# Kernel optimization log

Hardware: AMD Instinct MI355X
Metric: run time of the kernel (lower is better)

The kernel has to match this reference:

```python
import jax, jax.numpy as jnp
import numpy as np

N = 500_000            # nodes
E = 16_000_000         # used edges (var edges); E_total = 2*E
EPS = 1e-5             # BatchNorm eps
SQRT_C = np.sqrt(2.0).astype(np.float32)  # out_channels=2


def setup_inputs() -> dict:
    key = jax.random.key(0)
    ks = jax.random.split(key, 20)
    w = lambda k, s: (jax.random.normal(k, s, jnp.float32) * 0.5)
    d = {}
    d["x"] = jax.random.normal(ks[0], (N, 2), jnp.float32)
    d["edge_index"] = jax.random.randint(ks[1], (2, 2 * E), 0, N, jnp.int32)
    d["edge_attr"] = jax.random.normal(ks[2], (2 * E, 2), jnp.float32)
    d["mask"] = (jax.random.uniform(ks[3], (N,)) < 0.5).astype(jnp.float32)
    # TransformerConv(2,2,edge_dim=2,heads=1) params
    d["Wq"], d["bq"] = w(ks[4], (2, 2)), w(ks[5], (2,))
    d["Wk"], d["bk"] = w(ks[6], (2, 2)), w(ks[7], (2,))
    d["Wv"], d["bv"] = w(ks[8], (2, 2)), w(ks[9], (2,))
    d["We"] = w(ks[10], (2, 2))               # lin_edge, bias=False
    d["Wskip"], d["bskip"] = w(ks[11], (2, 2)), w(ks[12], (2,))
    # BatchNorm(2) affine params
    d["gamma"], d["beta"] = jnp.ones((2,), jnp.float32), jnp.zeros((2,), jnp.float32)
    # final Linear(2,1)
    d["Wf"], d["bf"] = w(ks[13], (1, 2)), w(ks[14], (1,))
    return d


def _transformer_conv(x, src, dst, ea, Wq, bq, Wk, bk, Wv, bv, We, Wskip, bskip):
    # PyG TransformerConv, heads=1, concat=True, root_weight=True, beta=False
    q = x @ Wq.T + bq                       # [N,2]
    k = x @ Wk.T + bk                       # [N,2]
    v = x @ Wv.T + bv                       # [N,2]
    e = ea @ We.T                           # [E,2]
    k_j = k[src] + e                        # [E,2]
    alpha = jnp.sum(q[dst] * k_j, axis=1) / SQRT_C  # [E]
    # segment softmax over destination nodes
    m = jax.ops.segment_max(alpha, dst, num_segments=N)          # -inf for empty
    m = jnp.where(jnp.isfinite(m), m, 0.0)
    a = jnp.exp(alpha - m[dst])
    s = jax.ops.segment_sum(a, dst, num_segments=N)
    wgt = a / jnp.where(s[dst] > 0, s[dst], 1.0)                 # [E]
    msg = (v[src] + e) * wgt[:, None]                            # [E,2]
    out = jax.ops.segment_sum(msg, dst, num_segments=N)          # [N,2]
    return out + x @ Wskip.T + bskip


def _neighbor_max(x, src, dst, ea_clause):
    # vectorized form of the per-node Python loop (scatter-max)
    s = jnp.sum(x[src] * ea_clause, axis=1)                      # [E]
    seg = jax.ops.segment_max(s, dst, num_segments=N)            # [N]
    deg = jax.ops.segment_sum(jnp.ones_like(s), dst, num_segments=N)
    has = deg > 0
    mx = jnp.where(has, seg, 0.0)
    stacked = jnp.stack([mx, 1.0 - mx], axis=1)                  # [N,2]
    return jnp.where(has[:, None], stacked, x)


def reference(x, edge_index, edge_attr, mask, Wq, bq, Wk, bk, Wv, bv, We,
              Wskip, bskip, gamma, beta, Wf, bf):
    ei = edge_index[:, 1::2]        # var_index = odd columns
    ea = edge_attr[1::2]            # var edge attrs
    ea_clause = edge_attr[0::2]     # clause edge attrs
    src, dst = ei[0], ei[1]
    h = _transformer_conv(x, src, dst, ea, Wq, bq, Wk, bk, Wv, bv, We, Wskip, bskip)
    # BatchNorm1d, training-mode batch statistics (biased var)
    mu = jnp.mean(h, axis=0)
    var = jnp.mean((h - mu) ** 2, axis=0)
    h = (h - mu) / jnp.sqrt(var + EPS) * gamma + beta
    # softmax over node dim (dim=0)
    h = jax.nn.softmax(h, axis=0)
    h = _neighbor_max(h, src, dst, ea_clause)
    # iterations=1 -> extra loop body does not execute
    out = jnp.squeeze(h @ Wf.T + bf)       # [N]
    return out * mask
```

## Files before the change

### kernel.cpp

```cpp
#include <hip/hip_runtime.h>
#include <hip/hip_fp16.h>

#define NNODES 500000
#define NEDGES 16000000
#define NBLK 1024
#define EPB (NEDGES / NBLK)
#define BSH 11
#define BSZ 2048
#define NBKT 245
#define BDIM 256
#define CHUNK 2048
#define KPC (CHUNK / 256)
#define CTH 1024

typedef unsigned long long u64;
typedef unsigned int u32;
typedef unsigned short u16;


__device__ __forceinline__ u32 fmap_ord(float x) {
    u32 u = __float_as_uint(x);
    return (u & 0x80000000u) ? ~u : (u | 0x80000000u);
}
__device__ __forceinline__ float funmap_ord(u32 u) {
    u32 bits = (u & 0x80000000u) ? (u ^ 0x80000000u) : ~u;
    return __uint_as_float(bits);
}

__device__ __forceinline__ void block_reduce_atomic4(float v0, float v1, float v2, float v3,
                                                     float* dst) {
    for (int off = 32; off > 0; off >>= 1) {
        v0 += __shfl_down(v0, off, 64);
        v1 += __shfl_down(v1, off, 64);
        v2 += __shfl_down(v2, off, 64);
        v3 += __shfl_down(v3, off, 64);
    }
    __shared__ float red[4][4];
    int lane = threadIdx.x & 63, wid = threadIdx.x >> 6;
    if (lane == 0) { red[wid][0] = v0; red[wid][1] = v1; red[wid][2] = v2; red[wid][3] = v3; }
    __syncthreads();
    if (threadIdx.x < 4) {
        float t = red[0][threadIdx.x] + red[1][threadIdx.x] + red[2][threadIdx.x] + red[3][threadIdx.x];
        unsafeAtomicAdd(&dst[threadIdx.x], t);
    }
}

__device__ __forceinline__ void block_reduce_atomic4_w16(float v0, float v1, float v2, float v3,
                                                         float* dst) {
    for (int off = 32; off > 0; off >>= 1) {
        v0 += __shfl_down(v0, off, 64);
        v1 += __shfl_down(v1, off, 64);
        v2 += __shfl_down(v2, off, 64);
        v3 += __shfl_down(v3, off, 64);
    }
    __shared__ float red[16][4];
    int lane = threadIdx.x & 63, wid = threadIdx.x >> 6;
    if (lane == 0) { red[wid][0] = v0; red[wid][1] = v1; red[wid][2] = v2; red[wid][3] = v3; }
    __syncthreads();
    if (threadIdx.x < 4) {
        float t = 0.f;
        #pragma unroll
        for (int w = 0; w < 16; ++w) t += red[w][threadIdx.x];
        unsafeAtomicAdd(&dst[threadIdx.x], t);
    }
}


__global__ __launch_bounds__(64) void k_zero_accum(float* accum) {
    if (threadIdx.x < 16) accum[threadIdx.x] = 0.f;
}

__global__ __launch_bounds__(256) void k_node_prep(
    const float* __restrict__ x,
    const float* __restrict__ Wq, const float* __restrict__ bq,
    const float* __restrict__ Wk, const float* __restrict__ bk,
    const float* __restrict__ Wv, const float* __restrict__ bv,
    float2* __restrict__ q, float4* __restrict__ kv) {
    int i = blockIdx.x * blockDim.x + threadIdx.x;
    if (i >= NNODES) return;
    float2 xv = ((const float2*)x)[i];
    float q0 = fmaf(Wq[0], xv.x, fmaf(Wq[1], xv.y, bq[0]));
    float q1 = fmaf(Wq[2], xv.x, fmaf(Wq[3], xv.y, bq[1]));
    float k0 = fmaf(Wk[0], xv.x, fmaf(Wk[1], xv.y, bk[0]));
    float k1 = fmaf(Wk[2], xv.x, fmaf(Wk[3], xv.y, bk[1]));
    float v0 = fmaf(Wv[0], xv.x, fmaf(Wv[1], xv.y, bv[0]));
    float v1 = fmaf(Wv[2], xv.x, fmaf(Wv[3], xv.y, bv[1]));
    q[i] = make_float2(q0, q1);
    kv[i] = make_float4(k0, k1, v0, v1);
}

__global__ void k_ln_final(const float* __restrict__ gamma, const float* __restrict__ beta,
                           float* __restrict__ accum) {
    float n = (float)NNODES;
    float mu0 = accum[0] / n, mu1 = accum[1] / n;
    float var0 = accum[2] / n - mu0 * mu0;
    float var1 = accum[3] / n - mu1 * mu1;
    float sc0 = gamma[0] * rsqrtf(var0 + 1e-5f);
    float sc1 = gamma[1] * rsqrtf(var1 + 1e-5f);
    accum[8] = sc0;
    accum[9] = sc1;
    accum[10] = beta[0] - mu0 * sc0;
    accum[11] = beta[1] - mu1 * sc1;
}

__global__ __launch_bounds__(256) void k_softmax(
    const float2* __restrict__ h, float2* __restrict__ pp, float* __restrict__ accum) {
    int i = blockIdx.x * blockDim.x + threadIdx.x;
    float p0 = 0.f, p1 = 0.f;
    if (i < NNODES) {
        float sc0 = accum[8], sc1 = accum[9], sh0 = accum[10], sh1 = accum[11];
        float2 hv = h[i];
        p0 = __expf(fmaf(hv.x, sc0, sh0));
        p1 = __expf(fmaf(hv.y, sc1, sh1));
        pp[i] = make_float2(p0, p1);
    }
    block_reduce_atomic4(p0, p1, 0.f, 0.f, accum + 4);
}

__global__ void k_sm_final(float* __restrict__ accum) {
    accum[12] = 1.f / accum[4];
    accum[13] = 1.f / accum[5];
}


__global__ __launch_bounds__(256) void k_hist(const int2* __restrict__ dst2, u32* __restrict__ M) {
    __shared__ u32 hist[BDIM];
    if (threadIdx.x < BDIM) hist[threadIdx.x] = 0u;
    __syncthreads();
    int beg = blockIdx.x * EPB, end = beg + EPB;
    #pragma unroll 4
    for (int e = beg + threadIdx.x; e < end; e += 256)
        atomicAdd(&hist[dst2[e].y >> BSH], 1u);
    __syncthreads();
    u32* row = M + (size_t)blockIdx.x * BDIM;
    if (threadIdx.x < BDIM) row[threadIdx.x] = hist[threadIdx.x];
}

__global__ __launch_bounds__(256) void k_bucket_prefix(u32* __restrict__ M, u32* __restrict__ bucketTotal) {
    __shared__ u32 col[NBLK];
    int b = blockIdx.x;
    for (int j = threadIdx.x; j < NBLK; j += 256) col[j] = M[(size_t)j * BDIM + b];
    __syncthreads();
    if (threadIdx.x == 0) {
        u32 run = 0;
        for (int j = 0; j < NBLK; ++j) { u32 c = col[j]; col[j] = run; run += c; }
        bucketTotal[b] = run;
    }
    __syncthreads();
    for (int j = threadIdx.x; j < NBLK; j += 256) M[(size_t)j * BDIM + b] = col[j];
}

__global__ __launch_bounds__(256) void k_scan_serial(const u32* __restrict__ bucketTotal,
                                                     u32* __restrict__ bucketBase) {
    __shared__ u32 t[BDIM];
    __shared__ u32 o[BDIM + 1];
    if (threadIdx.x < BDIM) t[threadIdx.x] = bucketTotal[threadIdx.x];
    __syncthreads();
    if (threadIdx.x == 0) {
        u32 run = 0;
        for (int j = 0; j < BDIM; ++j) { o[j] = run; run += t[j]; }
        o[BDIM] = run;
    }
    __syncthreads();
    for (int j = threadIdx.x; j < BDIM + 1; j += 256) bucketBase[j] = o[j];
}


__global__ __launch_bounds__(256) void k_scatter_stg(
    const int2* __restrict__ src2, const int2* __restrict__ dst2,
    const float4* __restrict__ ea4, const float* __restrict__ We,
    const u32* __restrict__ M, const u32* __restrict__ bucketBase,
    float4* __restrict__ R) {
    __shared__ u32 hist[BDIM];
    __shared__ u32 lbase[BDIM];
    __shared__ u32 gcur[BDIM];
    __shared__ u32 wsum[4];
    __shared__ float4 buf[CHUNK];
    __shared__ u16 bkt[CHUNK];

    const u32* row = M + (size_t)blockIdx.x * BDIM;
    if (threadIdx.x < BDIM) gcur[threadIdx.x] = row[threadIdx.x] + bucketBase[threadIdx.x];
    float we00 = We[0], we01 = We[1], we10 = We[2], we11 = We[3];
    int beg = blockIdx.x * EPB;
    int lane = threadIdx.x & 63, wid = threadIdx.x >> 6;

    for (int c0 = 0; c0 < EPB; c0 += CHUNK) {
        int cn = min(CHUNK, EPB - c0);
        if (threadIdx.x < BDIM) hist[threadIdx.x] = 0u;
        __syncthreads();

        float4 recs[KPC]; u32 bks[KPC]; u32 rnk[KPC]; bool val[KPC];
        #pragma unroll
        for (int k = 0; k < KPC; ++k) {
            int tt = k * 256 + threadIdx.x;
            val[k] = tt < cn;
            if (val[k]) {
                int e = beg + c0 + tt;
                int si = src2[e].y;
                int di = dst2[e].y;
                float4 eav = ea4[e];
                float e0 = fmaf(we00, eav.z, we01 * eav.w);
                float e1 = fmaf(we10, eav.z, we11 * eav.w);
                __half2 hc = __floats2half2_rn(eav.x, eav.y);
                u32 b = (u32)di >> BSH;
                u32 idx = (u32)si | ((u32)(di & (BSZ - 1)) << 19);
                recs[k] = make_float4(__uint_as_float(idx), e0, e1,
                                      __uint_as_float(*(u32*)&hc));
                bks[k] = b;
                rnk[k] = atomicAdd(&hist[b], 1u);
            }
        }
        __syncthreads();

        u32 s = hist[threadIdx.x];
        u32 inc = s;
        #pragma unroll
        for (int d = 1; d < 64; d <<= 1) {
            u32 v = __shfl_up(inc, d, 64);
            if (lane >= d) inc += v;
        }
        if (lane == 63) wsum[wid] = inc;
        __syncthreads();
        u32 woff = 0;
        for (int w = 0; w < wid; ++w) woff += wsum[w];
        lbase[threadIdx.x] = woff + inc - s;
        __syncthreads();

        #pragma unroll
        for (int k = 0; k < KPC; ++k) {
            if (val[k]) {
                u32 p = lbase[bks[k]] + rnk[k];
                buf[p] = recs[k];
                bkt[p] = (u16)bks[k];
            }
        }
        __syncthreads();

        for (int j = threadIdx.x; j < cn; j += 256) {
            u32 b = bkt[j];
            R[(size_t)gcur[b] + (u32)j - lbase[b]] = buf[j];
        }
        __syncthreads();

        if (threadIdx.x < BDIM) gcur[threadIdx.x] += hist[threadIdx.x];
        __syncthreads();
    }
}

__global__ __launch_bounds__(CTH) void k_attn16(
    const float4* __restrict__ R,
    const u32* __restrict__ bucketBase, const u32* __restrict__ bucketTotal,
    const float4* __restrict__ kv, const float2* __restrict__ qp,
    const float* __restrict__ x,
    const float* __restrict__ Wskip, const float* __restrict__ bskip,
    float2* __restrict__ h, float* __restrict__ accum) {
    __shared__ float sA[BSZ], m0A[BSZ], m1A[BSZ];
    __shared__ float2 qT[BSZ];
    int b = blockIdx.x, base = b << BSH;
    for (int j = threadIdx.x; j < BSZ; j += CTH) {
        sA[j] = 0.f; m0A[j] = 0.f; m1A[j] = 0.f;
        int i = base + j;
        qT[j] = (i < NNODES) ? qp[i] : make_float2(0.f, 0.f);
    }
    __syncthreads();
    int beg = bucketBase[b], end = beg + bucketTotal[b];
    for (int idx = beg + threadIdx.x; idx < end; idx += CTH) {
        float4 r = R[idx];
        u32 rec = __float_as_uint(r.x);
        int si = rec & 0x7FFFFu;
        int li = rec >> 19;
        float4 kvv = kv[si];
        float2 qv = qT[li];
        float alpha = fmaf(qv.x, kvv.x + r.y, qv.y * (kvv.y + r.z)) * 0.70710678118654752f;
        float a = __expf(alpha);
        atomicAdd(&sA[li], a);
        atomicAdd(&m0A[li], a * (kvv.z + r.y));
        atomicAdd(&m1A[li], a * (kvv.w + r.z));
    }
    __syncthreads();
    float r0 = 0.f, r1 = 0.f, r2 = 0.f, r3 = 0.f;
    float w00 = Wskip[0], w01 = Wskip[1], w10 = Wskip[2], w11 = Wskip[3];
    float c0 = bskip[0], c1 = bskip[1];
    for (int j = threadIdx.x; j < BSZ; j += CTH) {
        int i = base + j;
        if (i < NNODES) {
            float2 xv = ((const float2*)x)[i];
            float s = sA[j];
            float inv = s > 0.f ? 1.f / s : 0.f;
            float h0 = fmaf(m0A[j], inv, fmaf(w00, xv.x, fmaf(w01, xv.y, c0)));
            float h1 = fmaf(m1A[j], inv, fmaf(w10, xv.x, fmaf(w11, xv.y, c1)));
            h[i] = make_float2(h0, h1);
            r0 += h0; r1 += h1; r2 += h0 * h0; r3 += h1 * h1;
        }
    }
    block_reduce_atomic4_w16(r0, r1, r2, r3, accum);
}

__global__ __launch_bounds__(CTH) void k_nmax16(
    const float4* __restrict__ R,
    const u32* __restrict__ bucketBase, const u32* __restrict__ bucketTotal,
    const float2* __restrict__ pp, const float* __restrict__ accum,
    const float* __restrict__ Wf, const float* __restrict__ bf,
    const float* __restrict__ mask, float* __restrict__ out) {
    __shared__ u32 mxA[BSZ];
    __shared__ float maskT[BSZ];
    int b = blockIdx.x, base = b << BSH;
    for (int j = threadIdx.x; j < BSZ; j += CTH) {
        mxA[j] = 0u;
        int i = base + j;
        maskT[j] = (i < NNODES) ? mask[i] : 0.f;
    }
    __syncthreads();
    float inv0 = accum[12], inv1 = accum[13];
    int beg = bucketBase[b], end = beg + bucketTotal[b];
    for (int idx = beg + threadIdx.x; idx < end; idx += CTH) {
        float4 r = R[idx];
        u32 rec = __float_as_uint(r.x);
        int li = rec >> 19;
        if (maskT[li] == 0.f) continue;
        int si = rec & 0x7FFFFu;
        u32 hcbits = __float_as_uint(r.w);
        __half2 hc = *(__half2*)&hcbits;
        float2 cf = __half22float2(hc);
        float2 pv = pp[si];
        float sE = fmaf(pv.x * inv0, cf.x, pv.y * inv1 * cf.y);
        atomicMax(&mxA[li], fmap_ord(sE));
    }
    __syncthreads();
    float wf0 = Wf[0], wf1 = Wf[1], bb = bf[0];
    for (int j = threadIdx.x; j < BSZ; j += CTH) {
        int i = base + j;
        if (i >= NNODES) continue;
        u32 m = mxA[j];
        float h0, h1;
        if (m != 0u) { float v = funmap_ord(m); h0 = v; h1 = 1.f - v; }
        else { float2 pv = pp[i]; h0 = pv.x * inv0; h1 = pv.y * inv1; }
        out[i] = fmaf(wf0, h0, fmaf(wf1, h1, bb)) * maskT[j];
    }
}


__global__ __launch_bounds__(256) void k_init_f(float* s, float* msg, u32* mxb, float* accum) {
    int i = blockIdx.x * blockDim.x + threadIdx.x;
    if (i < NNODES) { s[i] = 0.f; mxb[i] = 0u; }
    if (i < 2 * NNODES) msg[i] = 0.f;
    if (i < 16) accum[i] = 0.f;
}

__global__ __launch_bounds__(256) void k_edge_attn_f(
    const int* __restrict__ ei, const float* __restrict__ ea,
    const float* __restrict__ We,
    const float2* __restrict__ q, const float4* __restrict__ kv,
    float* __restrict__ s, float* __restrict__ msg) {
    int e = blockIdx.x * blockDim.x + threadIdx.x;
    if (e >= NEDGES) return;
    float we00 = We[0], we01 = We[1], we10 = We[2], we11 = We[3];
    int si = ((const int2*)ei)[e].y;
    int di = ((const int2*)(ei + 2 * NEDGES))[e].y;
    float2 eav = ((const float2*)ea)[2 * e + 1];
    float4 kvv = kv[si];
    float2 qv = q[di];
    float e0 = fmaf(we00, eav.x, we01 * eav.y);
    float e1 = fmaf(we10, eav.x, we11 * eav.y);
    float alpha = fmaf(qv.x, kvv.x + e0, qv.y * (kvv.y + e1)) * 0.70710678118654752f;
    float a = __expf(alpha);
    unsafeAtomicAdd(&s[di], a);
    unsafeAtomicAdd(&msg[2 * di], a * (kvv.z + e0));
    unsafeAtomicAdd(&msg[2 * di + 1], a * (kvv.w + e1));
}

__global__ __launch_bounds__(256) void k_node_h_f(
    const float* __restrict__ x,
    const float* __restrict__ Wskip, const float* __restrict__ bskip,
    const float* __restrict__ s, float* __restrict__ msg, float* __restrict__ accum) {
    int i = blockIdx.x * blockDim.x + threadIdx.x;
    float h0 = 0.f, h1 = 0.f;
    if (i < NNODES) {
        float2 xv = ((const float2*)x)[i];
        float sk0 = fmaf(Wskip[0], xv.x, fmaf(Wskip[1], xv.y, bskip[0]));
        float sk1 = fmaf(Wskip[2], xv.x, fmaf(Wskip[3], xv.y, bskip[1]));
        float sv = s[i];
        float inv = sv > 0.f ? 1.f / sv : 0.f;
        h0 = fmaf(msg[2 * i], inv, sk0);
        h1 = fmaf(msg[2 * i + 1], inv, sk1);
        msg[2 * i] = h0;
        msg[2 * i + 1] = h1;
    }
    block_reduce_atomic4(h0, h1, h0 * h0, h1 * h1, accum);
}

__global__ __launch_bounds__(256) void k_edge_nmax_f(
    const int* __restrict__ ei, const float* __restrict__ ea,
    const float2* __restrict__ pp, const float* __restrict__ accum,
    u32* __restrict__ mxb) {
    int e = blockIdx.x * blockDim.x + threadIdx.x;
    if (e >= NEDGES) return;
    float inv0 = accum[12], inv1 = accum[13];
    int si = ((const int2*)ei)[e].y;
    int di = ((const int2*)(ei + 2 * NEDGES))[e].y;
    float2 c = ((const float2*)ea)[2 * e];
    float2 pv = pp[si];
    float sE = fmaf(pv.x * inv0, c.x, pv.y * inv1 * c.y);
    atomicMax(&mxb[di], fmap_ord(sE));
}

__global__ __launch_bounds__(256) void k_final_f(
    const u32* __restrict__ mxb, const float2* __restrict__ pp,
    const float* __restrict__ accum,
    const float* __restrict__ Wf, const float* __restrict__ bf,
    const float* __restrict__ mask, float* __restrict__ out) {
    int i = blockIdx.x * blockDim.x + threadIdx.x;
    if (i >= NNODES) return;
    u32 m = mxb[i];
    float h0, h1;
    if (m != 0u) {
        float v = funmap_ord(m);
        h0 = v;
        h1 = 1.f - v;
    } else {
        float2 pv = pp[i];
        h0 = pv.x * accum[12];
        h1 = pv.y * accum[13];
    }
    out[i] = fmaf(Wf[0], h0, fmaf(Wf[1], h1, bf[0])) * mask[i];
}


extern "C" void kernel_launch(void* const* d_in, const int* in_sizes, int n_in,
                              void* d_out, int out_size, void* d_ws, size_t ws_size,
                              hipStream_t stream) {
    const float* x     = (const float*)d_in[0];
    const int*   ei    = (const int*)d_in[1];
    const float* ea    = (const float*)d_in[2];
    const float* mask  = (const float*)d_in[3];
    const float* Wq    = (const float*)d_in[4];
    const float* bq    = (const float*)d_in[5];
    const float* Wk    = (const float*)d_in[6];
    const float* bk    = (const float*)d_in[7];
    const float* Wv    = (const float*)d_in[8];
    const float* bv    = (const float*)d_in[9];
    const float* We    = (const float*)d_in[10];
    const float* Wskip = (const float*)d_in[11];
    const float* bskip = (const float*)d_in[12];
    const float* gamma = (const float*)d_in[13];
    const float* beta  = (const float*)d_in[14];
    const float* Wf    = (const float*)d_in[15];
    const float* bf    = (const float*)d_in[16];
    float* out = (float*)d_out;

    const size_t N = NNODES;
    const size_t E = NEDGES;
    const int B = 256;
    const int gridN = (NNODES + B - 1) / B;

    const int2*   src2 = (const int2*)ei;
    const int2*   dst2 = (const int2*)(ei + 2 * NEDGES);
    const float4* ea4  = (const float4*)ea;

    size_t need16 = 16 * N
                  + 16 * E
                  + 8 * N
                  + 8 * N
                  + 8 * N
                  + 4 * (size_t)NBLK * BDIM
                  + 4 * BDIM
                  + 4 * (BDIM + 16)
                  + 64;

    if (ws_size >= need16) {
        char* base = (char*)d_ws;
        float4* kv = (float4*)base;                 base += 16 * N;
        float4* R  = (float4*)base;                 base += 16 * E;
        float2* q  = (float2*)base;                 base += 8 * N;
        float2* h  = (float2*)base;                 base += 8 * N;
        float2* p  = (float2*)base;                 base += 8 * N;
        u32*    M  = (u32*)base;                    base += 4 * (size_t)NBLK * BDIM;
        u32*    bT = (u32*)base;                    base += 4 * BDIM;
        u32*    bB = (u32*)base;                    base += 4 * (BDIM + 16);
        float*  accum = (float*)base;

        k_zero_accum<<<1, 64, 0, stream>>>(accum);
        k_node_prep<<<gridN, B, 0, stream>>>(x, Wq, bq, Wk, bk, Wv, bv, q, kv);
        k_hist<<<NBLK, B, 0, stream>>>(dst2, M);
        k_bucket_prefix<<<BDIM, B, 0, stream>>>(M, bT);
        k_scan_serial<<<1, B, 0, stream>>>(bT, bB);
        k_scatter_stg<<<NBLK, B, 0, stream>>>(src2, dst2, ea4, We, M, bB, R);
        k_attn16<<<NBKT, CTH, 0, stream>>>(R, bB, bT, kv, q, x, Wskip, bskip, h, accum);
        k_ln_final<<<1, 1, 0, stream>>>(gamma, beta, accum);
        k_softmax<<<gridN, B, 0, stream>>>(h, p, accum);
        k_sm_final<<<1, 1, 0, stream>>>(accum);
        k_nmax16<<<NBKT, CTH, 0, stream>>>(R, bB, bT, p, accum, Wf, bf, mask, out);
    } else {
        float*  q   = (float*)d_ws;
        float*  kvf = q + 2 * N;
        float*  s   = kvf + 4 * N;
        float*  msg = s + N;
        u32*    mxb = (u32*)(msg + 2 * N);
        float*  accum = (float*)(mxb + N);
        int grid2N = (int)((2 * N + B - 1) / B);
        int gridE  = (NEDGES + B - 1) / B;

        k_init_f<<<grid2N, B, 0, stream>>>(s, msg, mxb, accum);
        k_node_prep<<<gridN, B, 0, stream>>>(x, Wq, bq, Wk, bk, Wv, bv, (float2*)q, (float4*)kvf);
        k_edge_attn_f<<<gridE, B, 0, stream>>>(ei, ea, We, (const float2*)q, (const float4*)kvf, s, msg);
        k_node_h_f<<<gridN, B, 0, stream>>>(x, Wskip, bskip, s, msg, accum);
        k_ln_final<<<1, 1, 0, stream>>>(gamma, beta, accum);
        k_softmax<<<gridN, B, 0, stream>>>((const float2*)msg, (float2*)q, accum);
        k_sm_final<<<1, 1, 0, stream>>>(accum);
        k_edge_nmax_f<<<gridE, B, 0, stream>>>(ei, ea, (const float2*)q, accum, mxb);
        k_final_f<<<gridN, B, 0, stream>>>(mxb, (const float2*)q, accum, Wf, bf, mask, out);
    }
}
```

Measured before the change: 664.0 us.

## Compute attention weights during scatter and split edge records for nmax pass

The exp-weighted attention terms are now computed per edge in the scatter kernel, which gathers q[dst] and kv[src] itself, and it writes precomputed (a, a*m0, a*m1) records. The attention kernel then only does shared-memory atomic accumulation. A separate 8-byte record array carries the index and half-precision clause attributes, so the neighbor-max pass reads half the bytes. In exchange the scatter kernel does random q gathers over the whole node range instead of a bucket-local shared-memory table, and it writes an extra 8 bytes per edge. The workspace also grows by 8 bytes per edge, which could push execution onto the fallback path if the workspace is small.

Result: slower. 1.015 ms (+52.9%).

```diff
diff --git a/kernel.cpp b/kernel.cpp
--- a/kernel.cpp
+++ b/kernel.cpp
@@ -166,16 +166,18 @@
 }
 
 
-__global__ __launch_bounds__(256) void k_scatter_stg(
+__global__ __launch_bounds__(256) void k_scatter_fused(
     const int2* __restrict__ src2, const int2* __restrict__ dst2,
     const float4* __restrict__ ea4, const float* __restrict__ We,
+    const float2* __restrict__ qp, const float4* __restrict__ kvp,
     const u32* __restrict__ M, const u32* __restrict__ bucketBase,
-    float4* __restrict__ R) {
+    float4* __restrict__ R1, uint2* __restrict__ R2) {
     __shared__ u32 hist[BDIM];
     __shared__ u32 lbase[BDIM];
     __shared__ u32 gcur[BDIM];
     __shared__ u32 wsum[4];
-    __shared__ float4 buf[CHUNK];
+    __shared__ float4 buf1[CHUNK];
+    __shared__ uint2 buf2[CHUNK];
     __shared__ u16 bkt[CHUNK];
 
     const u32* row = M + (size_t)blockIdx.x * BDIM;
@@ -189,7 +191,7 @@
         if (threadIdx.x < BDIM) hist[threadIdx.x] = 0u;
         __syncthreads();
 
-        float4 recs[KPC]; u32 bks[KPC]; u32 rnk[KPC]; bool val[KPC];
+        float4 r1[KPC]; uint2 r2[KPC]; u32 bks[KPC]; u32 rnk[KPC]; bool val[KPC];
         #pragma unroll
         for (int k = 0; k < KPC; ++k) {
             int tt = k * 256 + threadIdx.x;
@@ -201,11 +203,17 @@
                 float4 eav = ea4[e];
                 float e0 = fmaf(we00, eav.z, we01 * eav.w);
                 float e1 = fmaf(we10, eav.z, we11 * eav.w);
+                float4 kvv = kvp[si];
+                float2 qv = qp[di];
+                float alpha = fmaf(qv.x, kvv.x + e0, qv.y * (kvv.y + e1)) * 0.70710678118654752f;
+                float a = __expf(alpha);
+                float am0 = a * (kvv.z + e0);
+                float am1 = a * (kvv.w + e1);
+                u32 b = (u32)di >> BSH;
+                u32 lisi = (u32)si | ((u32)(di & (BSZ - 1)) << 19);
                 __half2 hc = __floats2half2_rn(eav.x, eav.y);
-                u32 b = (u32)di >> BSH;
-                u32 idx = (u32)si | ((u32)(di & (BSZ - 1)) << 19);
-                recs[k] = make_float4(__uint_as_float(idx), e0, e1,
-                                      __uint_as_float(*(u32*)&hc));
+                r1[k] = make_float4(__uint_as_float(lisi), a, am0, am1);
+                r2[k] = make_uint2(lisi, *(u32*)&hc);
                 bks[k] = b;
                 rnk[k] = atomicAdd(&hist[b], 1u);
             }
@@ -230,7 +238,8 @@
         for (int k = 0; k < KPC; ++k) {
             if (val[k]) {
                 u32 p = lbase[bks[k]] + rnk[k];
-                buf[p] = recs[k];
+                buf1[p] = r1[k];
+                buf2[p] = r2[k];
                 bkt[p] = (u16)bks[k];
             }
         }
@@ -238,7 +247,9 @@
 
         for (int j = threadIdx.x; j < cn; j += 256) {
             u32 b = bkt[j];
-            R[(size_t)gcur[b] + (u32)j - lbase[b]] = buf[j];
+            u32 off = gcur[b] + (u32)j - lbase[b];
+            R1[(size_t)off] = buf1[j];
+            R2[(size_t)off] = buf2[j];
         }
         __syncthreads();
 
@@ -248,34 +259,24 @@
 }
 
 __global__ __launch_bounds__(CTH) void k_attn16(
-    const float4* __restrict__ R,
+    const float4* __restrict__ R1,
     const u32* __restrict__ bucketBase, const u32* __restrict__ bucketTotal,
-    const float4* __restrict__ kv, const float2* __restrict__ qp,
     const float* __restrict__ x,
     const float* __restrict__ Wskip, const float* __restrict__ bskip,
     float2* __restrict__ h, float* __restrict__ accum) {
     __shared__ float sA[BSZ], m0A[BSZ], m1A[BSZ];
-    __shared__ float2 qT[BSZ];
     int b = blockIdx.x, base = b << BSH;
     for (int j = threadIdx.x; j < BSZ; j += CTH) {
         sA[j] = 0.f; m0A[j] = 0.f; m1A[j] = 0.f;
-        int i = base + j;
-        qT[j] = (i < NNODES) ? qp[i] : make_float2(0.f, 0.f);
     }
     __syncthreads();
     int beg = bucketBase[b], end = beg + bucketTotal[b];
     for (int idx = beg + threadIdx.x; idx < end; idx += CTH) {
-        float4 r = R[idx];
-        u32 rec = __float_as_uint(r.x);
-        int si = rec & 0x7FFFFu;
-        int li = rec >> 19;
-        float4 kvv = kv[si];
-        float2 qv = qT[li];
-        float alpha = fmaf(qv.x, kvv.x + r.y, qv.y * (kvv.y + r.z)) * 0.70710678118654752f;
-        float a = __expf(alpha);
-        atomicAdd(&sA[li], a);
-        atomicAdd(&m0A[li], a * (kvv.z + r.y));
-        atomicAdd(&m1A[li], a * (kvv.w + r.z));
+        float4 r = R1[idx];
+        int li = (int)(__float_as_uint(r.x) >> 19);
+        atomicAdd(&sA[li], r.y);
+        atomicAdd(&m0A[li], r.z);
+        atomicAdd(&m1A[li], r.w);
     }
     __syncthreads();
     float r0 = 0.f, r1 = 0.f, r2 = 0.f, r3 = 0.f;
@@ -297,7 +298,7 @@
 }
 
 __global__ __launch_bounds__(CTH) void k_nmax16(
-    const float4* __restrict__ R,
+    const uint2* __restrict__ R2,
     const u32* __restrict__ bucketBase, const u32* __restrict__ bucketTotal,
     const float2* __restrict__ pp, const float* __restrict__ accum,
     const float* __restrict__ Wf, const float* __restrict__ bf,
@@ -314,13 +315,11 @@
     float inv0 = accum[12], inv1 = accum[13];
     int beg = bucketBase[b], end = beg + bucketTotal[b];
     for (int idx = beg + threadIdx.x; idx < end; idx += CTH) {
-        float4 r = R[idx];
-        u32 rec = __float_as_uint(r.x);
-        int li = rec >> 19;
+        uint2 r = R2[idx];
+        int li = (int)(r.x >> 19);
         if (maskT[li] == 0.f) continue;
-        int si = rec & 0x7FFFFu;
-        u32 hcbits = __float_as_uint(r.w);
-        __half2 hc = *(__half2*)&hcbits;
+        int si = (int)(r.x & 0x7FFFFu);
+        __half2 hc = *(__half2*)&r.y;
         float2 cf = __half22float2(hc);
         float2 pv = pp[si];
         float sE = fmaf(pv.x * inv0, cf.x, pv.y * inv1 * cf.y);
@@ -457,20 +456,22 @@
     const int2*   dst2 = (const int2*)(ei + 2 * NEDGES);
     const float4* ea4  = (const float4*)ea;
 
-    size_t need16 = 16 * N
-                  + 16 * E
-                  + 8 * N
-                  + 8 * N
-                  + 8 * N
-                  + 4 * (size_t)NBLK * BDIM
-                  + 4 * BDIM
-                  + 4 * (BDIM + 16)
-                  + 64;
-
-    if (ws_size >= need16) {
+    size_t need = 16 * N
+                + 16 * E
+                + 8 * E
+                + 8 * N
+                + 8 * N
+                + 8 * N
+                + 4 * (size_t)NBLK * BDIM
+                + 4 * BDIM
+                + 4 * (BDIM + 16)
+                + 64;
+
+    if (ws_size >= need) {
         char* base = (char*)d_ws;
         float4* kv = (float4*)base;                 base += 16 * N;
-        float4* R  = (float4*)base;                 base += 16 * E;
+        float4* R1 = (float4*)base;                 base += 16 * E;
+        uint2*  R2 = (uint2*)base;                  base += 8 * E;
         float2* q  = (float2*)base;                 base += 8 * N;
         float2* h  = (float2*)base;                 base += 8 * N;
         float2* p  = (float2*)base;                 base += 8 * N;
@@ -484,12 +485,12 @@
         k_hist<<<NBLK, B, 0, stream>>>(dst2, M);
         k_bucket_prefix<<<BDIM, B, 0, stream>>>(M, bT);
         k_scan_serial<<<1, B, 0, stream>>>(bT, bB);
-        k_scatter_stg<<<NBLK, B, 0, stream>>>(src2, dst2, ea4, We, M, bB, R);
-        k_attn16<<<NBKT, CTH, 0, stream>>>(R, bB, bT, kv, q, x, Wskip, bskip, h, accum);
+        k_scatter_fused<<<NBLK, B, 0, stream>>>(src2, dst2, ea4, We, q, kv, M, bB, R1, R2);
+        k_attn16<<<NBKT, CTH, 0, stream>>>(R1, bB, bT, x, Wskip, bskip, h, accum);
         k_ln_final<<<1, 1, 0, stream>>>(gamma, beta, accum);
         k_softmax<<<gridN, B, 0, stream>>>(h, p, accum);
         k_sm_final<<<1, 1, 0, stream>>>(accum);
-        k_nmax16<<<NBKT, CTH, 0, stream>>>(R, bB, bT, p, accum, Wf, bf, mask, out);
+        k_nmax16<<<NBKT, CTH, 0, stream>>>(R2, bB, bT, p, accum, Wf, bf, mask, out);
     } else {
         float*  q   = (float*)d_ws;
         float*  kvf = q + 2 * N;
```
